# Kernel tuning notes

Measured on AMD Instinct MI355X. Metric: run time of the kernel, lower is better.

## Reference

```python
import jax, jax.numpy as jnp
import numpy as np

N_NODES = 50000
N_EDGES = 600000
HIDDEN = 128
N_LAYERS = 5


def setup_inputs() -> dict:
    key = jax.random.key(0)
    ks = jax.random.split(key, 4)
    x = jax.random.normal(ks[0], (N_NODES, HIDDEN), dtype=jnp.float32)
    edge_index = jax.random.randint(ks[1], (2, N_EDGES), 0, N_NODES, dtype=jnp.int64)
    scale = 1.0 / np.sqrt(HIDDEN)
    Wl = jax.random.normal(ks[2], (N_LAYERS, HIDDEN, HIDDEN), dtype=jnp.float32) * scale
    Wr = jax.random.normal(ks[3], (N_LAYERS, HIDDEN, HIDDEN), dtype=jnp.float32) * scale
    b = jnp.zeros((N_LAYERS, HIDDEN), dtype=jnp.float32)
    return {"x": x, "edge_index": edge_index, "Wl": Wl, "Wr": Wr, "b": b}


def _sage_conv(x, src, dst, deg_inv, Wl, Wr, b):
    # mean aggregation of source-node features at destination nodes
    msg = x[src]                                          # [E, d] gather
    agg = jax.ops.segment_sum(msg, dst, num_segments=N_NODES)  # [N, d]
    mean = agg * deg_inv                                  # [N, d]
    # PyG SAGEConv: lin_l(aggregated) + lin_r(root), bias on lin_l
    return mean @ Wl.T + b + x @ Wr.T


def reference(x, edge_index, Wl, Wr, b):
    src, dst = edge_index[0], edge_index[1]
    deg = jax.ops.segment_sum(jnp.ones((N_EDGES,), x.dtype), dst, num_segments=N_NODES)
    deg_inv = (1.0 / jnp.maximum(deg, 1.0))[:, None]      # avoid div-by-zero for isolated nodes
    h = x
    for l in range(N_LAYERS):
        h = _sage_conv(h, src, dst, deg_inv, Wl[l], Wr[l], b[l])
        if l < N_LAYERS - 1:
            h = jax.nn.relu(h)
    return h
```

## Files before the change

kernel.cpp:

```cpp
#include <hip/hip_runtime.h>

#define N_NODES 50000
#define N_EDGES 600000
#define HID 128
#define N_LAYERS 5
#define SCAN_BLK 256
#define N_SCAN_BLOCKS ((N_NODES + SCAN_BLK - 1) / SCAN_BLK)
#define NH ((size_t)N_NODES * HID)

typedef unsigned int u32;
typedef _Float16 half8 __attribute__((ext_vector_type(8)));
typedef _Float16 half4 __attribute__((ext_vector_type(4)));
typedef float f32x4 __attribute__((ext_vector_type(4)));
typedef u32 u32x8 __attribute__((ext_vector_type(8)));

union PK { u32 u; _Float16 h[2]; };

__device__ inline u32 pack_split(float v) {
    PK r;
    r.h[0] = (_Float16)v;
    r.h[1] = (_Float16)(v - (float)r.h[0]);
    return r.u;
}
__device__ inline float unpack_sum(u32 p) {
    PK r; r.u = p;
    return (float)r.h[0] + (float)r.h[1];
}


__global__ void deg_count(const int* __restrict__ dst, int* __restrict__ deg) {
    int e = blockIdx.x * blockDim.x + threadIdx.x;
    if (e < N_EDGES) atomicAdd(&deg[dst[e]], 1);
}

__global__ __launch_bounds__(SCAN_BLK) void deg_reduce(const int* __restrict__ deg,
                                                       int* __restrict__ block_sums) {
    __shared__ int s[SCAN_BLK];
    int i = blockIdx.x * SCAN_BLK + threadIdx.x;
    int v = (i < N_NODES) ? deg[i] : 0;
    s[threadIdx.x] = v;
    __syncthreads();
    for (int off = SCAN_BLK / 2; off > 0; off >>= 1) {
        if (threadIdx.x < off) s[threadIdx.x] += s[threadIdx.x + off];
        __syncthreads();
    }
    if (threadIdx.x == 0) block_sums[blockIdx.x] = s[0];
}

__global__ __launch_bounds__(SCAN_BLK) void scan_partials(const int* __restrict__ block_sums,
                                                          int* __restrict__ block_off) {
    __shared__ int s[SCAN_BLK];
    int t = threadIdx.x;
    int v = (t < N_SCAN_BLOCKS) ? block_sums[t] : 0;
    s[t] = v;
    __syncthreads();
    for (int off = 1; off < SCAN_BLK; off <<= 1) {
        int u = (t >= off) ? s[t - off] : 0;
        __syncthreads();
        s[t] += u;
        __syncthreads();
    }
    if (t < N_SCAN_BLOCKS) block_off[t] = s[t] - v;
}

__global__ __launch_bounds__(SCAN_BLK) void scan_write(const int* __restrict__ deg,
        const int* __restrict__ block_off, int* __restrict__ row_ptr,
        int* __restrict__ cursor, float* __restrict__ deg_inv) {
    __shared__ int s[SCAN_BLK];
    int t = threadIdx.x;
    int i = blockIdx.x * SCAN_BLK + t;
    int v = (i < N_NODES) ? deg[i] : 0;
    s[t] = v;
    __syncthreads();
    for (int off = 1; off < SCAN_BLK; off <<= 1) {
        int u = (t >= off) ? s[t - off] : 0;
        __syncthreads();
        s[t] += u;
        __syncthreads();
    }
    int excl = s[t] - v + block_off[blockIdx.x];
    if (i < N_NODES) {
        row_ptr[i] = excl;
        cursor[i]  = excl;
        deg_inv[i] = 1.0f / (float)max(v, 1);
    }
    if (i == N_NODES) row_ptr[N_NODES] = excl;
}

__global__ void fill_csr(const int* __restrict__ src, const int* __restrict__ dst,
                         int* __restrict__ cursor, int* __restrict__ col) {
    int e = blockIdx.x * blockDim.x + threadIdx.x;
    if (e < N_EDGES) {
        int d = dst[e];
        int pos = atomicAdd(&cursor[d], 1);
        col[pos] = src[e];
    }
}


__global__ void split_sep(const float* __restrict__ src,
                          _Float16* __restrict__ hi, _Float16* __restrict__ lo, int n4) {
    int i = blockIdx.x * blockDim.x + threadIdx.x;
    if (i >= n4) return;
    float4 v = *(const float4*)(src + (size_t)i * 4);
    half4 h, l;
    h.x = (_Float16)v.x; l.x = (_Float16)(v.x - (float)h.x);
    h.y = (_Float16)v.y; l.y = (_Float16)(v.y - (float)h.y);
    h.z = (_Float16)v.z; l.z = (_Float16)(v.z - (float)h.z);
    h.w = (_Float16)v.w; l.w = (_Float16)(v.w - (float)h.w);
    *(half4*)(hi + (size_t)i * 4) = h;
    *(half4*)(lo + (size_t)i * 4) = l;
}

__global__ void split_pk(const float* __restrict__ src, u32* __restrict__ dst, int n4) {
    int i = blockIdx.x * blockDim.x + threadIdx.x;
    if (i >= n4) return;
    float4 v = *(const float4*)(src + (size_t)i * 4);
    uint4 r;
    r.x = pack_split(v.x); r.y = pack_split(v.y);
    r.z = pack_split(v.z); r.w = pack_split(v.w);
    *(uint4*)(dst + (size_t)i * 4) = r;
}


__global__ __launch_bounds__(256) void aggregate_w64(const u32* __restrict__ hp,
        const int* __restrict__ row_ptr, const int* __restrict__ col,
        const float* __restrict__ deg_inv, u32* __restrict__ mp) {
    int wave = threadIdx.x >> 6;
    int lane = threadIdx.x & 63;
    int node = blockIdx.x * 4 + wave;
    if (node >= N_NODES) return;
    int beg = row_ptr[node], end = row_ptr[node + 1];
    int deg = end - beg;
    const int slot = lane >> 5;
    const int fo   = (lane & 31) * 4;
    float a0 = 0.f, a1 = 0.f, a2 = 0.f, a3 = 0.f;

    for (int base = 0; base < deg; base += 64) {
        int cnt = deg - base; if (cnt > 64) cnt = 64;
        int p = beg + base + lane;
        int ci = col[(p < end) ? p : (end - 1)];
        int e = 0;
        for (; e + 3 < cnt; e += 4) {
            int s0 = __shfl(ci, e + slot, 64);
            int s1 = __shfl(ci, e + 2 + slot, 64);
            uint4 v0 = *(const uint4*)(hp + (size_t)s0 * HID + fo);
            uint4 v1 = *(const uint4*)(hp + (size_t)s1 * HID + fo);
            a0 += unpack_sum(v0.x) + unpack_sum(v1.x);
            a1 += unpack_sum(v0.y) + unpack_sum(v1.y);
            a2 += unpack_sum(v0.z) + unpack_sum(v1.z);
            a3 += unpack_sum(v0.w) + unpack_sum(v1.w);
        }
        for (; e < cnt; e += 2) {
            int idx = e + slot;
            int s0 = __shfl(ci, (idx < cnt) ? idx : 0, 64);
            if (idx < cnt) {
                uint4 v0 = *(const uint4*)(hp + (size_t)s0 * HID + fo);
                a0 += unpack_sum(v0.x);
                a1 += unpack_sum(v0.y);
                a2 += unpack_sum(v0.z);
                a3 += unpack_sum(v0.w);
            }
        }
    }
    a0 += __shfl_xor(a0, 32, 64);
    a1 += __shfl_xor(a1, 32, 64);
    a2 += __shfl_xor(a2, 32, 64);
    a3 += __shfl_xor(a3, 32, 64);
    if (lane < 32) {
        float di = deg_inv[node];
        uint4 r;
        r.x = pack_split(a0 * di);
        r.y = pack_split(a1 * di);
        r.z = pack_split(a2 * di);
        r.w = pack_split(a3 * di);
        *(uint4*)(mp + (size_t)node * HID + fo) = r;
    }
}


__device__ inline void unpk8(u32x8 p, half8& hi, half8& lo) {
    #pragma unroll
    for (int i = 0; i < 8; ++i) {
        PK t; t.u = p[i];
        hi[i] = t.h[0];
        lo[i] = t.h[1];
    }
}

__global__ __launch_bounds__(512, 2) void gemm_mfma(
        const u32* __restrict__ mean_pk, const u32* __restrict__ h_pk,
        const _Float16* __restrict__ Wlh, const _Float16* __restrict__ Wll,
        const _Float16* __restrict__ Wrh, const _Float16* __restrict__ Wrl,
        const float* __restrict__ bias,
        u32* __restrict__ out_pk, float* __restrict__ out_f32, int final_layer) {
    __shared__ char Wlds[131072];
    const int t    = threadIdx.x;
    const int lane = t & 63;
    const int w    = t >> 6;
    const int jr   = lane & 15;
    const int q    = lane >> 4;

    #pragma unroll
    for (int i = 0; i < 4; ++i) {
        int gi = t + i * 512;
        int j = gi >> 4, p = gi & 15;
        int dstb = j * 256 + (p ^ (j & 7)) * 16;
        int srci = j * HID + p * 8;
        *(half8*)&Wlds[0 * 32768 + dstb] = *(const half8*)(Wlh + srci);
        *(half8*)&Wlds[1 * 32768 + dstb] = *(const half8*)(Wll + srci);
        *(half8*)&Wlds[2 * 32768 + dstb] = *(const half8*)(Wrh + srci);
        *(half8*)&Wlds[3 * 32768 + dstb] = *(const half8*)(Wrl + srci);
    }
    __syncthreads();

    const int base0 = blockIdx.x * 256 + w * 32;
    int r0 = base0 + jr;      if (r0 > N_NODES - 1) r0 = N_NODES - 1;
    int r1 = base0 + 16 + jr; if (r1 > N_NODES - 1) r1 = N_NODES - 1;
    const int ko = q * 8;

    f32x4 acc0[8], acc1[8];
    #pragma unroll
    for (int jt = 0; jt < 8; ++jt) {
        acc0[jt] = (f32x4)(0.f);
        acc1[jt] = (f32x4)(0.f);
    }

    #pragma unroll 2
    for (int kk = 0; kk < 4; ++kk) {
        const size_t a0 = (size_t)r0 * HID + kk * 32 + ko;
        const size_t a1 = (size_t)r1 * HID + kk * 32 + ko;
        u32x8 mp0 = *(const u32x8*)(mean_pk + a0);
        u32x8 hp0 = *(const u32x8*)(h_pk   + a0);
        u32x8 mp1 = *(const u32x8*)(mean_pk + a1);
        u32x8 hp1 = *(const u32x8*)(h_pk   + a1);
        half8 mh0, ml0, hh0, hl0, mh1, ml1, hh1, hl1;
        unpk8(mp0, mh0, ml0); unpk8(hp0, hh0, hl0);
        unpk8(mp1, mh1, ml1); unpk8(hp1, hh1, hl1);
        #pragma unroll
        for (int jt = 0; jt < 8; ++jt) {
            int j  = jt * 16 + jr;
            int wb = j * 256 + (((kk * 4 + q) ^ (j & 7)) * 16);
            half8 wlh = *(const half8*)&Wlds[0 * 32768 + wb];
            half8 wll = *(const half8*)&Wlds[1 * 32768 + wb];
            half8 wrh = *(const half8*)&Wlds[2 * 32768 + wb];
            half8 wrl = *(const half8*)&Wlds[3 * 32768 + wb];
            acc0[jt] = __builtin_amdgcn_mfma_f32_16x16x32_f16(mh0, wlh, acc0[jt], 0, 0, 0);
            acc0[jt] = __builtin_amdgcn_mfma_f32_16x16x32_f16(ml0, wlh, acc0[jt], 0, 0, 0);
            acc0[jt] = __builtin_amdgcn_mfma_f32_16x16x32_f16(mh0, wll, acc0[jt], 0, 0, 0);
            acc0[jt] = __builtin_amdgcn_mfma_f32_16x16x32_f16(hh0, wrh, acc0[jt], 0, 0, 0);
            acc0[jt] = __builtin_amdgcn_mfma_f32_16x16x32_f16(hl0, wrh, acc0[jt], 0, 0, 0);
            acc0[jt] = __builtin_amdgcn_mfma_f32_16x16x32_f16(hh0, wrl, acc0[jt], 0, 0, 0);
            acc1[jt] = __builtin_amdgcn_mfma_f32_16x16x32_f16(mh1, wlh, acc1[jt], 0, 0, 0);
            acc1[jt] = __builtin_amdgcn_mfma_f32_16x16x32_f16(ml1, wlh, acc1[jt], 0, 0, 0);
            acc1[jt] = __builtin_amdgcn_mfma_f32_16x16x32_f16(mh1, wll, acc1[jt], 0, 0, 0);
            acc1[jt] = __builtin_amdgcn_mfma_f32_16x16x32_f16(hh1, wrh, acc1[jt], 0, 0, 0);
            acc1[jt] = __builtin_amdgcn_mfma_f32_16x16x32_f16(hl1, wrh, acc1[jt], 0, 0, 0);
            acc1[jt] = __builtin_amdgcn_mfma_f32_16x16x32_f16(hh1, wrl, acc1[jt], 0, 0, 0);
        }
    }

    float bv[8];
    #pragma unroll
    for (int jt = 0; jt < 8; ++jt) bv[jt] = bias[jt * 16 + jr];

    #pragma unroll
    for (int jt = 0; jt < 8; ++jt) {
        #pragma unroll
        for (int g = 0; g < 4; ++g) {
            int row = base0 + q * 4 + g;
            if (row < N_NODES) {
                float v = acc0[jt][g] + bv[jt];
                size_t idx = (size_t)row * HID + jt * 16 + jr;
                if (final_layer) out_f32[idx] = v;
                else             out_pk[idx] = pack_split(fmaxf(v, 0.f));
            }
            int row2 = base0 + 16 + q * 4 + g;
            if (row2 < N_NODES) {
                float v = acc1[jt][g] + bv[jt];
                size_t idx = (size_t)row2 * HID + jt * 16 + jr;
                if (final_layer) out_f32[idx] = v;
                else             out_pk[idx] = pack_split(fmaxf(v, 0.f));
            }
        }
    }
}


extern "C" void kernel_launch(void* const* d_in, const int* in_sizes, int n_in,
                              void* d_out, int out_size, void* d_ws, size_t ws_size,
                              hipStream_t stream) {
    const float* x    = (const float*)d_in[0];
    const int*   edge = (const int*)d_in[1];
    const float* Wl   = (const float*)d_in[2];
    const float* Wr   = (const float*)d_in[3];
    const float* bias = (const float*)d_in[4];
    float* out = (float*)d_out;

    u32* h_pk    = (u32*)d_ws;
    u32* mean_pk = h_pk + NH;
    _Float16* Wlh = (_Float16*)(mean_pk + NH);
    _Float16* Wll = Wlh + 81920;
    _Float16* Wrh = Wll + 81920;
    _Float16* Wrl = Wrh + 81920;
    float* deg_inv = (float*)(Wrl + 81920);
    int*   deg     = (int*)(deg_inv + N_NODES);
    int*   row_ptr = deg + N_NODES;
    int*   cursor  = row_ptr + (N_NODES + 1);
    int*   colarr  = cursor + N_NODES;
    int*   blk_sums = colarr + N_EDGES;
    int*   blk_off  = blk_sums + N_SCAN_BLOCKS;

    const int* src = edge;
    const int* dst = edge + N_EDGES;

    hipMemsetAsync(deg, 0, N_NODES * sizeof(int), stream);
    deg_count<<<(N_EDGES + 255) / 256, 256, 0, stream>>>(dst, deg);
    deg_reduce<<<N_SCAN_BLOCKS, SCAN_BLK, 0, stream>>>(deg, blk_sums);
    scan_partials<<<1, SCAN_BLK, 0, stream>>>(blk_sums, blk_off);
    scan_write<<<N_SCAN_BLOCKS, SCAN_BLK, 0, stream>>>(deg, blk_off, row_ptr,
                                                       cursor, deg_inv);
    fill_csr<<<(N_EDGES + 255) / 256, 256, 0, stream>>>(src, dst, cursor, colarr);

    split_sep<<<(20480 + 255) / 256, 256, 0, stream>>>(Wl, Wlh, Wll, 20480);
    split_sep<<<(20480 + 255) / 256, 256, 0, stream>>>(Wr, Wrh, Wrl, 20480);
    split_pk<<<(1638400 + 255) / 256, 256, 0, stream>>>(x, h_pk, 1638400);

    for (int l = 0; l < N_LAYERS; ++l) {
        aggregate_w64<<<(N_NODES + 3) / 4, 256, 0, stream>>>(
            h_pk, row_ptr, colarr, deg_inv, mean_pk);
        gemm_mfma<<<(N_NODES + 255) / 256, 512, 0, stream>>>(
            mean_pk, h_pk,
            Wlh + (size_t)l * 16384, Wll + (size_t)l * 16384,
            Wrh + (size_t)l * 16384, Wrl + (size_t)l * 16384,
            bias + (size_t)l * HID,
            h_pk, out, (l == N_LAYERS - 1) ? 1 : 0);
    }
}
```

Baseline: 402.9 us.

## Slice node features into 16-column planes and split GEMM weight loading into two phases

Stores packed node features in eight column-slice planes of 16 features each, so the aggregation kernel processes one slice per block. The goal is to make each slice's gathered working set small enough to sit in cache across the irregular neighbor reads. The GEMM reads and writes this sliced layout. It also halves its LDS footprint by loading the hi weights first and the lo weights second, with 128-row tiles and higher occupancy. In exchange, aggregation launches eight times as many blocks, each re-reading the CSR indices, and per-edge lane utilization drops for low-degree nodes.

```diff
diff --git a/kernel.cpp b/kernel.cpp
--- a/kernel.cpp
+++ b/kernel.cpp
@@ -7,6 +7,8 @@
 #define SCAN_BLK 256
 #define N_SCAN_BLOCKS ((N_NODES + SCAN_BLK - 1) / SCAN_BLK)
 #define NH ((size_t)N_NODES * HID)
+#define NSLICE 8
+#define SL_STRIDE ((size_t)N_NODES * 16)
 
 typedef unsigned int u32;
 typedef _Float16 half8 __attribute__((ext_vector_type(8)));
@@ -112,69 +114,62 @@
     *(half4*)(lo + (size_t)i * 4) = l;
 }
 
-__global__ void split_pk(const float* __restrict__ src, u32* __restrict__ dst, int n4) {
+__global__ void split_pk_sl(const float* __restrict__ src, u32* __restrict__ dst, int nq) {
     int i = blockIdx.x * blockDim.x + threadIdx.x;
-    if (i >= n4) return;
-    float4 v = *(const float4*)(src + (size_t)i * 4);
+    if (i >= nq) return;
+    int n = i >> 5;
+    int c = i & 31;
+    float4 v = *(const float4*)(src + (size_t)n * HID + c * 4);
     uint4 r;
     r.x = pack_split(v.x); r.y = pack_split(v.y);
     r.z = pack_split(v.z); r.w = pack_split(v.w);
-    *(uint4*)(dst + (size_t)i * 4) = r;
-}
-
-
-__global__ __launch_bounds__(256) void aggregate_w64(const u32* __restrict__ hp,
+    int slice = c >> 2, rem = (c & 3) * 4;
+    *(uint4*)(dst + (size_t)slice * SL_STRIDE + (size_t)n * 16 + rem) = r;
+}
+
+
+__global__ __launch_bounds__(256) void aggregate_sl(const u32* __restrict__ hp,
         const int* __restrict__ row_ptr, const int* __restrict__ col,
         const float* __restrict__ deg_inv, u32* __restrict__ mp) {
-    int wave = threadIdx.x >> 6;
-    int lane = threadIdx.x & 63;
-    int node = blockIdx.x * 4 + wave;
+    const int wave  = threadIdx.x >> 6;
+    const int lane  = threadIdx.x & 63;
+    const int slice = blockIdx.x & 7;
+    const int node  = (blockIdx.x >> 3) * 4 + wave;
     if (node >= N_NODES) return;
+    const u32* hsl = hp + (size_t)slice * SL_STRIDE;
     int beg = row_ptr[node], end = row_ptr[node + 1];
     int deg = end - beg;
-    const int slot = lane >> 5;
-    const int fo   = (lane & 31) * 4;
+    const int eslot = lane >> 2;
+    const int rem   = (lane & 3) * 4;
     float a0 = 0.f, a1 = 0.f, a2 = 0.f, a3 = 0.f;
 
-    for (int base = 0; base < deg; base += 64) {
-        int cnt = deg - base; if (cnt > 64) cnt = 64;
-        int p = beg + base + lane;
+    for (int base = 0; base < deg; base += 16) {
+        int cnt = deg - base; if (cnt > 16) cnt = 16;
+        int p = beg + base + (lane & 15);
         int ci = col[(p < end) ? p : (end - 1)];
-        int e = 0;
-        for (; e + 3 < cnt; e += 4) {
-            int s0 = __shfl(ci, e + slot, 64);
-            int s1 = __shfl(ci, e + 2 + slot, 64);
-            uint4 v0 = *(const uint4*)(hp + (size_t)s0 * HID + fo);
-            uint4 v1 = *(const uint4*)(hp + (size_t)s1 * HID + fo);
-            a0 += unpack_sum(v0.x) + unpack_sum(v1.x);
-            a1 += unpack_sum(v0.y) + unpack_sum(v1.y);
-            a2 += unpack_sum(v0.z) + unpack_sum(v1.z);
-            a3 += unpack_sum(v0.w) + unpack_sum(v1.w);
+        int srcn = __shfl(ci, eslot, 64);
+        if (eslot < cnt) {
+            uint4 v = *(const uint4*)(hsl + (size_t)srcn * 16 + rem);
+            a0 += unpack_sum(v.x); a1 += unpack_sum(v.y);
+            a2 += unpack_sum(v.z); a3 += unpack_sum(v.w);
         }
-        for (; e < cnt; e += 2) {
-            int idx = e + slot;
-            int s0 = __shfl(ci, (idx < cnt) ? idx : 0, 64);
-            if (idx < cnt) {
-                uint4 v0 = *(const uint4*)(hp + (size_t)s0 * HID + fo);
-                a0 += unpack_sum(v0.x);
-                a1 += unpack_sum(v0.y);
-                a2 += unpack_sum(v0.z);
-                a3 += unpack_sum(v0.w);
-            }
-        }
-    }
-    a0 += __shfl_xor(a0, 32, 64);
-    a1 += __shfl_xor(a1, 32, 64);
-    a2 += __shfl_xor(a2, 32, 64);
-    a3 += __shfl_xor(a3, 32, 64);
-    if (lane < 32) {
+    }
+    a0 += __shfl_xor(a0, 4, 64);  a1 += __shfl_xor(a1, 4, 64);
+    a2 += __shfl_xor(a2, 4, 64);  a3 += __shfl_xor(a3, 4, 64);
+    a0 += __shfl_xor(a0, 8, 64);  a1 += __shfl_xor(a1, 8, 64);
+    a2 += __shfl_xor(a2, 8, 64);  a3 += __shfl_xor(a3, 8, 64);
+    a0 += __shfl_xor(a0, 16, 64); a1 += __shfl_xor(a1, 16, 64);
+    a2 += __shfl_xor(a2, 16, 64); a3 += __shfl_xor(a3, 16, 64);
+    a0 += __shfl_xor(a0, 32, 64); a1 += __shfl_xor(a1, 32, 64);
+    a2 += __shfl_xor(a2, 32, 64); a3 += __shfl_xor(a3, 32, 64);
+    if (lane < 4) {
         float di = deg_inv[node];
         uint4 r;
         r.x = pack_split(a0 * di);
         r.y = pack_split(a1 * di);
         r.z = pack_split(a2 * di);
         r.w = pack_split(a3 * di);
-        *(uint4*)(mp + (size_t)node * HID + fo) = r;
+        *(uint4*)(mp + (size_t)slice * SL_STRIDE + (size_t)node * 16 + rem) = r;
     }
 }
 
@@ -187,76 +182,90 @@
         lo[i] = t.h[1];
     }
 }
-
-__global__ __launch_bounds__(512, 2) void gemm_mfma(
+__device__ inline void unpk8_hi(u32x8 p, half8& hi) {
+    #pragma unroll
+    for (int i = 0; i < 8; ++i) {
+        PK t; t.u = p[i];
+        hi[i] = t.h[0];
+    }
+}
+
+__global__ __launch_bounds__(512, 4) void gemm_mfma(
         const u32* __restrict__ mean_pk, const u32* __restrict__ h_pk,
         const _Float16* __restrict__ Wlh, const _Float16* __restrict__ Wll,
         const _Float16* __restrict__ Wrh, const _Float16* __restrict__ Wrl,
         const float* __restrict__ bias,
         u32* __restrict__ out_pk, float* __restrict__ out_f32, int final_layer) {
-    __shared__ char Wlds[131072];
+    __shared__ char Wlds[65536];
     const int t    = threadIdx.x;
     const int lane = t & 63;
     const int w    = t >> 6;
     const int jr   = lane & 15;
     const int q    = lane >> 4;
 
+    const int basew = blockIdx.x * 128 + w * 16;
+    int r0 = basew + jr; if (r0 > N_NODES - 1) r0 = N_NODES - 1;
+
+    f32x4 accL[8], accR[8];
+    #pragma unroll
+    for (int jt = 0; jt < 8; ++jt) { accL[jt] = (f32x4)(0.f); accR[jt] = (f32x4)(0.f); }
+
     #pragma unroll
     for (int i = 0; i < 4; ++i) {
         int gi = t + i * 512;
         int j = gi >> 4, p = gi & 15;
-        int dstb = j * 256 + (p ^ (j & 7)) * 16;
+        int dstb = j * 256 + ((p ^ (j & 7)) * 16);
         int srci = j * HID + p * 8;
-        *(half8*)&Wlds[0 * 32768 + dstb] = *(const half8*)(Wlh + srci);
-        *(half8*)&Wlds[1 * 32768 + dstb] = *(const half8*)(Wll + srci);
-        *(half8*)&Wlds[2 * 32768 + dstb] = *(const half8*)(Wrh + srci);
-        *(half8*)&Wlds[3 * 32768 + dstb] = *(const half8*)(Wrl + srci);
-    }
-    __syncthreads();
-
-    const int base0 = blockIdx.x * 256 + w * 32;
-    int r0 = base0 + jr;      if (r0 > N_NODES - 1) r0 = N_NODES - 1;
-    int r1 = base0 + 16 + jr; if (r1 > N_NODES - 1) r1 = N_NODES - 1;
-    const int ko = q * 8;
-
-    f32x4 acc0[8], acc1[8];
-    #pragma unroll
-    for (int jt = 0; jt < 8; ++jt) {
-        acc0[jt] = (f32x4)(0.f);
-        acc1[jt] = (f32x4)(0.f);
-    }
-
+        *(half8*)&Wlds[dstb]         = *(const half8*)(Wlh + srci);
+        *(half8*)&Wlds[32768 + dstb] = *(const half8*)(Wrh + srci);
+    }
+    __syncthreads();
     #pragma unroll 2
     for (int kk = 0; kk < 4; ++kk) {
-        const size_t a0 = (size_t)r0 * HID + kk * 32 + ko;
-        const size_t a1 = (size_t)r1 * HID + kk * 32 + ko;
-        u32x8 mp0 = *(const u32x8*)(mean_pk + a0);
-        u32x8 hp0 = *(const u32x8*)(h_pk   + a0);
-        u32x8 mp1 = *(const u32x8*)(mean_pk + a1);
-        u32x8 hp1 = *(const u32x8*)(h_pk   + a1);
-        half8 mh0, ml0, hh0, hl0, mh1, ml1, hh1, hl1;
-        unpk8(mp0, mh0, ml0); unpk8(hp0, hh0, hl0);
-        unpk8(mp1, mh1, ml1); unpk8(hp1, hh1, hl1);
+        size_t a = ((size_t)(2 * kk + (q >> 1)) * N_NODES + r0) * 16 + (q & 1) * 8;
+        u32x8 mp8 = *(const u32x8*)(mean_pk + a);
+        u32x8 hp8 = *(const u32x8*)(h_pk + a);
+        half8 mh, ml, hh, hl;
+        unpk8(mp8, mh, ml); unpk8(hp8, hh, hl);
         #pragma unroll
         for (int jt = 0; jt < 8; ++jt) {
             int j  = jt * 16 + jr;
             int wb = j * 256 + (((kk * 4 + q) ^ (j & 7)) * 16);
-            half8 wlh = *(const half8*)&Wlds[0 * 32768 + wb];
-            half8 wll = *(const half8*)&Wlds[1 * 32768 + wb];
-            half8 wrh = *(const half8*)&Wlds[2 * 32768 + wb];
-            half8 wrl = *(const half8*)&Wlds[3 * 32768 + wb];
-            acc0[jt] = __builtin_amdgcn_mfma_f32_16x16x32_f16(mh0, wlh, acc0[jt], 0, 0, 0);
-            acc0[jt] = __builtin_amdgcn_mfma_f32_16x16x32_f16(ml0, wlh, acc0[jt], 0, 0, 0);
-            acc0[jt] = __builtin_amdgcn_mfma_f32_16x16x32_f16(mh0, wll, acc0[jt], 0, 0, 0);
-            acc0[jt] = __builtin_amdgcn_mfma_f32_16x16x32_f16(hh0, wrh, acc0[jt], 0, 0, 0);
-            acc0[jt] = __builtin_amdgcn_mfma_f32_16x16x32_f16(hl0, wrh, acc0[jt], 0, 0, 0);
-            acc0[jt] = __builtin_amdgcn_mfma_f32_16x16x32_f16(hh0, wrl, acc0[jt], 0, 0, 0);
-            acc1[jt] = __builtin_amdgcn_mfma_f32_16x16x32_f16(mh1, wlh, acc1[jt], 0, 0, 0);
-            acc1[jt] = __builtin_amdgcn_mfma_f32_16x16x32_f16(ml1, wlh, acc1[jt], 0, 0, 0);
-            acc1[jt] = __builtin_amdgcn_mfma_f32_16x16x32_f16(mh1, wll, acc1[jt], 0, 0, 0);
-            acc1[jt] = __builtin_amdgcn_mfma_f32_16x16x32_f16(hh1, wrh, acc1[jt], 0, 0, 0);
-            acc1[jt] = __builtin_amdgcn_mfma_f32_16x16x32_f16(hl1, wrh, acc1[jt], 0, 0, 0);
-            acc1[jt] = __builtin_amdgcn_mfma_f32_16x16x32_f16(hh1, wrl, acc1[jt], 0, 0, 0);
+            half8 wl = *(const half8*)&Wlds[wb];
+            half8 wr = *(const half8*)&Wlds[32768 + wb];
+            accL[jt] = __builtin_amdgcn_mfma_f32_16x16x32_f16(mh, wl, accL[jt], 0, 0, 0);
+            accL[jt] = __builtin_amdgcn_mfma_f32_16x16x32_f16(ml, wl, accL[jt], 0, 0, 0);
+            accR[jt] = __builtin_amdgcn_mfma_f32_16x16x32_f16(hh, wr, accR[jt], 0, 0, 0);
+            accR[jt] = __builtin_amdgcn_mfma_f32_16x16x32_f16(hl, wr, accR[jt], 0, 0, 0);
+        }
+    }
+    __syncthreads();
+
+    #pragma unroll
+    for (int i = 0; i < 4; ++i) {
+        int gi = t + i * 512;
+        int j = gi >> 4, p = gi & 15;
+        int dstb = j * 256 + ((p ^ (j & 7)) * 16);
+        int srci = j * HID + p * 8;
+        *(half8*)&Wlds[dstb]         = *(const half8*)(Wll + srci);
+        *(half8*)&Wlds[32768 + dstb] = *(const half8*)(Wrl + srci);
+    }
+    __syncthreads();
+    #pragma unroll 2
+    for (int kk = 0; kk < 4; ++kk) {
+        size_t a = ((size_t)(2 * kk + (q >> 1)) * N_NODES + r0) * 16 + (q & 1) * 8;
+        u32x8 mp8 = *(const u32x8*)(mean_pk + a);
+        u32x8 hp8 = *(const u32x8*)(h_pk + a);
+        half8 mh, hh;
+        unpk8_hi(mp8, mh); unpk8_hi(hp8, hh);
+        #pragma unroll
+        for (int jt = 0; jt < 8; ++jt) {
+            int j  = jt * 16 + jr;
+            int wb = j * 256 + (((kk * 4 + q) ^ (j & 7)) * 16);
+            half8 wl = *(const half8*)&Wlds[wb];
+            half8 wr = *(const half8*)&Wlds[32768 + wb];
+            accL[jt] = __builtin_amdgcn_mfma_f32_16x16x32_f16(mh, wl, accL[jt], 0, 0, 0);
+            accR[jt] = __builtin_amdgcn_mfma_f32_16x16x32_f16(hh, wr, accR[jt], 0, 0, 0);
         }
     }
 
@@ -268,19 +277,15 @@
     for (int jt = 0; jt < 8; ++jt) {
         #pragma unroll
         for (int g = 0; g < 4; ++g) {
-            int row = base0 + q * 4 + g;
+            int row = basew + q * 4 + g;
             if (row < N_NODES) {
-                float v = acc0[jt][g] + bv[jt];
-                size_t idx = (size_t)row * HID + jt * 16 + jr;
-                if (final_layer) out_f32[idx] = v;
-                else             out_pk[idx] = pack_split(fmaxf(v, 0.f));
-            }
-            int row2 = base0 + 16 + q * 4 + g;
-            if (row2 < N_NODES) {
-                float v = acc1[jt][g] + bv[jt];
-                size_t idx = (size_t)row2 * HID + jt * 16 + jr;
-                if (final_layer) out_f32[idx] = v;
-                else             out_pk[idx] = pack_split(fmaxf(v, 0.f));
+                float v = accL[jt][g] + accR[jt][g] + bv[jt];
+                if (final_layer) {
+                    out_f32[(size_t)row * HID + jt * 16 + jr] = v;
+                } else {
+                    out_pk[((size_t)jt * N_NODES + row) * 16 + jr] =
+                        pack_split(fmaxf(v, 0.f));
+                }
             }
         }
     }
@@ -324,12 +329,15 @@
 
     split_sep<<<(20480 + 255) / 256, 256, 0, stream>>>(Wl, Wlh, Wll, 20480);
     split_sep<<<(20480 + 255) / 256, 256, 0, stream>>>(Wr, Wrh, Wrl, 20480);
-    split_pk<<<(1638400 + 255) / 256, 256, 0, stream>>>(x, h_pk, 1638400);
+    split_pk_sl<<<(1600000 + 255) / 256, 256, 0, stream>>>(x, h_pk, 1600000);
+
+    const int agg_blocks = ((N_NODES + 3) / 4) * NSLICE;
+    const int gemm_blocks = (N_NODES + 127) / 128;
 
     for (int l = 0; l < N_LAYERS; ++l) {
-        aggregate_w64<<<(N_NODES + 3) / 4, 256, 0, stream>>>(
+        aggregate_sl<<<agg_blocks, 256, 0, stream>>>(
             h_pk, row_ptr, colarr, deg_inv, mean_pk);
-        gemm_mfma<<<(N_NODES + 255) / 256, 512, 0, stream>>>(
+        gemm_mfma<<<gemm_blocks, 512, 0, stream>>>(
             mean_pk, h_pk,
             Wlh + (size_t)l * 16384, Wll + (size_t)l * 16384,
             Wrh + (size_t)l * 16384, Wrl + (size_t)l * 16384,
```

New measurement: 708.6 us. +75.9%, slower.
